# Optimization experiments

Hardware: AMD Instinct MI355X
Metric: run time of the kernel (lower is better)

The kernel has to match this reference:

```python
import jax, jax.numpy as jnp
import numpy as np

P_MIN = 0.8        # minimum cumulative probability mass kept per row
THRESHOLD = 1e-10  # drop matches with probability below this
EPS = 1e-6         # distance clamp (matches dist.clamp(min=1e-6) in backward)

B, N, M, D = 4, 4096, 4096, 3


def setup_inputs() -> dict:
    key = jax.random.key(0)
    kx, ky = jax.random.split(key)
    x = jax.random.normal(kx, (B, N, D), dtype=jnp.float32)
    y = jax.random.normal(ky, (B, M, D), dtype=jnp.float32)
    return {"x": x, "y": y}


def _pairwise_dist(x, y):
    # ||x_i - y_j|| via Gram trick; avoids materializing [B,N,M,D] diff tensor.
    sq = (
        jnp.sum(x * x, axis=-1)[:, :, None]
        + jnp.sum(y * y, axis=-1)[:, None, :]
        - 2.0 * jnp.einsum("bnd,bmd->bnm", x, y)
    )
    return jnp.sqrt(jnp.maximum(sq, EPS * EPS))  # [B, N, M]


def _sparse_match_weights(d):
    # Row-wise soft matching probabilities over targets j.
    p = jax.nn.softmax(-d, axis=-1)  # [B, N, M]
    # Keep the most-probable entries per row until cumulative mass reaches P_MIN
    # (the dense, jit-friendly equivalent of the COO compaction in the kernel).
    order = jnp.argsort(-p, axis=-1)
    p_sorted = jnp.take_along_axis(p, order, axis=-1)
    csum = jnp.cumsum(p_sorted, axis=-1)
    keep_sorted = (csum - p_sorted) < P_MIN  # include entry that crosses P_MIN
    inv = jnp.argsort(order, axis=-1)
    keep = jnp.take_along_axis(keep_sorted, inv, axis=-1)
    return jnp.where(keep & (p > THRESHOLD), p, 0.0)  # sparse COO values, dense layout


def reference(x, y):
    d = _pairwise_dist(x, y)                     # [B, N, M]
    w = jax.lax.stop_gradient(_sparse_match_weights(d))  # weights are constants in bwd
    loss = jnp.sum(w * d)                        # scalar matching loss
    return loss
```

## Files before the change

kernel.cpp:

```cpp
#include <hip/hip_runtime.h>


#define MCOLS 4096
#define KPT   64
#define WPB   4
#define P_MIN 0.8f

template <int CTRL, int RM, int BM, bool BC>
__device__ __forceinline__ float dpp_mov0(float x) {
    return __int_as_float(__builtin_amdgcn_update_dpp(
        0, __float_as_int(x), CTRL, RM, BM, BC));
}
__device__ __forceinline__ float dppSum(float v) {
    v += dpp_mov0<0x111, 0xF, 0xF, true >(v);
    v += dpp_mov0<0x112, 0xF, 0xF, true >(v);
    v += dpp_mov0<0x114, 0xF, 0xF, true >(v);
    v += dpp_mov0<0x118, 0xF, 0xF, true >(v);
    v += dpp_mov0<0x142, 0xA, 0xF, false>(v);
    v += dpp_mov0<0x143, 0xC, 0xF, false>(v);
    return __int_as_float(__builtin_amdgcn_readlane(__float_as_int(v), 63));
}
__device__ __forceinline__ float dppMax(float v) {
    v = fmaxf(v, dpp_mov0<0x111, 0xF, 0xF, true >(v));
    v = fmaxf(v, dpp_mov0<0x112, 0xF, 0xF, true >(v));
    v = fmaxf(v, dpp_mov0<0x114, 0xF, 0xF, true >(v));
    v = fmaxf(v, dpp_mov0<0x118, 0xF, 0xF, true >(v));
    v = fmaxf(v, dpp_mov0<0x142, 0xA, 0xF, false>(v));
    v = fmaxf(v, dpp_mov0<0x143, 0xC, 0xF, false>(v));
    return __int_as_float(__builtin_amdgcn_readlane(__float_as_int(v), 63));
}

__global__ __launch_bounds__(WPB * 64) void apml_row_wave(
        const float* __restrict__ x, const float* __restrict__ y,
        float* __restrict__ out) {
    __shared__ __align__(16) float scomp[WPB * 256];
    __shared__ float wacc[WPB];

    const int tid  = threadIdx.x;
    const int wid  = tid >> 6;
    const int lane = tid & 63;
    const int row  = blockIdx.x * WPB + wid;
    const int b    = row >> 12;

    const float x0 = x[row * 3 + 0];
    const float x1 = x[row * 3 + 1];
    const float x2 = x[row * 3 + 2];
    const float* yb = y + (size_t)b * MCOLS * 3;

    float p[KPT];
    float zl = 0.0f, pml = 0.0f;
    #pragma unroll
    for (int k = 0; k < KPT; ++k) {
        const int j = k * 64 + lane;
        const float y0 = yb[j * 3 + 0];
        const float y1 = yb[j * 3 + 1];
        const float y2 = yb[j * 3 + 2];
        const float dx = x0 - y0, dy = x1 - y1, dz = x2 - y2;
        const float sq = fmaxf(dx * dx + dy * dy + dz * dz, 1e-12f);
        const float pk = __expf(-sqrtf(sq));
        p[k] = pk;
        zl  += pk;
        pml  = fmaxf(pml, pk);
    }
    const float Z    = dppSum(zl);
    const float pmax = dppMax(pml);
    const float target = P_MIN * Z;
    const float pTop = __uint_as_float(__float_as_uint(pmax) + 1u);

    float ssl = 0.0f, ssh = pTop;
    {
        float eGl = 16.0f * dppSum(p[0] + p[1] + p[2] + p[3]);
        float eGh = 0.0f;
        for (int it = 0; it < 5; ++it) {
            float s;
            if (it & 1) {
                s = 0.5f * (ssl + ssh);
            } else {
                const float den = fmaxf(eGl - eGh, 1e-30f);
                s = ssl + (ssh - ssl) * ((eGl - target) / den);
            }
            if (!(s > ssl && s < ssh)) s = 0.5f * (ssl + ssh);
            if (!(s > ssl && s < ssh)) break;
            float m = 0.0f;
            #pragma unroll
            for (int q = 0; q < 4; ++q) m += (p[q] >= s) ? p[q] : 0.0f;
            m = 16.0f * dppSum(m);
            if (m >= target) { ssl = s; eGl = m; }
            else             { ssh = s; eGh = m; }
        }
    }

    float sl = 0.0f, sh = pTop;
    float Gl = Z,    Gh = 0.0f;
    int   Cl = MCOLS, Ch = 0;

    for (int it = 0; it < 12 && (Cl - Ch) > 256; ++it) {
        float s;
        if      (it == 0) s = ssl;
        else if (it == 1) s = ssh;
        else if (it & 1)  s = 0.5f * (sl + sh);
        else {
            const float den = fmaxf(Gl - Gh, 1e-30f);
            s = sl + (sh - sl) * ((Gl - target) / den);
        }
        if (!(s > sl && s < sh)) s = 0.5f * (sl + sh);
        if (!(s > sl && s < sh)) break;

        float m = 0.0f;
        int   c = 0;
        #pragma unroll
        for (int k = 0; k < KPT; ++k) {
            const bool ge = (p[k] >= s);
            m += ge ? p[k] : 0.0f;
            c += (int)__popcll(__ballot(ge));
        }
        m = dppSum(m);
        if (m >= target) { sl = s; Gl = m; Cl = c; }
        else             { sh = s; Gh = m; Ch = c; }
    }

    int C = 0;
    #pragma unroll
    for (int k = 0; k < KPT; ++k) {
        const bool band = (p[k] >= sl) && (p[k] < sh);
        const unsigned long long mk = __ballot(band);
        if (band) {
            const unsigned mlo = (unsigned)mk, mhi = (unsigned)(mk >> 32);
            const int within = __builtin_amdgcn_mbcnt_hi(
                                   mhi, __builtin_amdgcn_mbcnt_lo(mlo, 0));
            const int pos = C + within;
            if (pos < 256) scomp[wid * 256 + pos] = p[k];
        }
        C += (int)__popcll(mk);
    }
    __builtin_amdgcn_s_waitcnt(0);
    float cp[4];
    bool  cv[4];
    #pragma unroll
    for (int q = 0; q < 4; ++q) {
        const int idx = q * 64 + lane;
        cv[q] = (idx < C) && (idx < 256);
        cp[q] = cv[q] ? scomp[wid * 256 + idx] : 0.0f;
    }

    float pstar, mb = 0.0f;
    int   cnt = 1;
    bool  haveTie;

    if (C > 256) {
        pstar = (sl > 0.0f) ? __uint_as_float(__float_as_uint(sl) - 1u) : 0.0f;
        haveTie = false;
    } else {
        float lo_s = sl, hi_s = sh, lo_G = Gl, hi_G = Gh;
        int   lo_C = Cl, hi_C = Ch;
        for (int it = 0; it < 10 && (lo_C - hi_C) > 2; ++it) {
            float s;
            if (it & 1) {
                s = 0.5f * (lo_s + hi_s);
            } else {
                const float den = fmaxf(lo_G - hi_G, 1e-30f);
                s = lo_s + (hi_s - lo_s) * ((lo_G - target) / den);
            }
            if (!(s > lo_s && s < hi_s)) s = 0.5f * (lo_s + hi_s);
            if (!(s > lo_s && s < hi_s)) break;

            float m = 0.0f;
            int   c = Ch;
            #pragma unroll
            for (int q = 0; q < 4; ++q) {
                const bool ge = cv[q] && (cp[q] >= s);
                m += ge ? cp[q] : 0.0f;
                c += (int)__popcll(__ballot(ge));
            }
            m = Gh + dppSum(m);
            if (m >= target) { lo_s = s; lo_G = m; lo_C = c; }
            else             { hi_s = s; hi_G = m; hi_C = c; }
        }

        float scur = hi_s, M = hi_G;
        bool ok = false;
        pstar = lo_s;
        for (int e = 0; e < 16; ++e) {
            float vl = 0.0f;
            #pragma unroll
            for (int q = 0; q < 4; ++q)
                vl = fmaxf(vl, (cv[q] && cp[q] < scur) ? cp[q] : 0.0f);
            const float v = dppMax(vl);
            if (!(v > 0.0f)) break;
            int cvn = 0;
            #pragma unroll
            for (int q = 0; q < 4; ++q)
                cvn += (int)__popcll(__ballot(cv[q] && (cp[q] == v)));
            const float Mn = M + v * (float)cvn;
            if (Mn >= target) { pstar = v; mb = M; cnt = cvn; ok = true; break; }
            M = Mn; scur = v;
        }
        haveTie = ok;
        if (!ok) {
            pstar = (lo_s > 0.0f) ? __uint_as_float(__float_as_uint(lo_s) - 1u)
                                  : 0.0f;
        }
    }

    float spd = 0.0f;
    #pragma unroll
    for (int k = 0; k < KPT; ++k) {
        const float t = (p[k] > pstar) ? p[k] : 1.0f;
        spd += t * (-__logf(t));
    }
    spd = dppSum(spd);

    if (lane == 0) {
        float tie = 0.0f;
        if (haveTie) {
            const float R = (target - mb) / pstar;
            int q = (int)ceilf(R);
            if (q < 1) q = 1;
            if (q > cnt) q = cnt;
            tie = (float)q * pstar * (-__logf(pstar));
        }
        wacc[wid] = (spd + tie) / Z;
    }
    __syncthreads();
    if (tid == 0) {
        atomicAdd(out, wacc[0] + wacc[1] + wacc[2] + wacc[3]);
    }
}

extern "C" void kernel_launch(void* const* d_in, const int* in_sizes, int n_in,
                              void* d_out, int out_size, void* d_ws, size_t ws_size,
                              hipStream_t stream) {
    const float* x = (const float*)d_in[0];
    const float* y = (const float*)d_in[1];
    float* out = (float*)d_out;

    const int nrows = in_sizes[0] / 3;
    const int nblocks = nrows / WPB;

    hipMemsetAsync(out, 0, sizeof(float), stream);
    apml_row_wave<<<nblocks, WPB * 64, 0, stream>>>(x, y, out);
}
```

Before: 166.9 us.

## Batch initial threshold probes, split reductions into ILP chains, replace atomics with reduce kernel

The first two threshold probes of the mass search now run in a single pass over the 64 per-lane values, with both dual DPP sums interleaved. The remaining probe loop and the running max use four independent accumulators to shorten dependency chains. The global atomicAdd plus memset is replaced by per-block partials written to workspace and a separate single-block reduction kernel, which adds a second launch but removes atomic contention and the memset. The intent is fewer serialized reduction steps per row and cheaper final accumulation.

```diff
diff --git a/kernel.cpp b/kernel.cpp
--- a/kernel.cpp
+++ b/kernel.cpp
@@ -20,6 +20,16 @@
     v += dpp_mov0<0x143, 0xC, 0xF, false>(v);
     return __int_as_float(__builtin_amdgcn_readlane(__float_as_int(v), 63));
 }
+__device__ __forceinline__ void dppSum2(float& a, float& b) {
+    a += dpp_mov0<0x111, 0xF, 0xF, true >(a); b += dpp_mov0<0x111, 0xF, 0xF, true >(b);
+    a += dpp_mov0<0x112, 0xF, 0xF, true >(a); b += dpp_mov0<0x112, 0xF, 0xF, true >(b);
+    a += dpp_mov0<0x114, 0xF, 0xF, true >(a); b += dpp_mov0<0x114, 0xF, 0xF, true >(b);
+    a += dpp_mov0<0x118, 0xF, 0xF, true >(a); b += dpp_mov0<0x118, 0xF, 0xF, true >(b);
+    a += dpp_mov0<0x142, 0xA, 0xF, false>(a); b += dpp_mov0<0x142, 0xA, 0xF, false>(b);
+    a += dpp_mov0<0x143, 0xC, 0xF, false>(a); b += dpp_mov0<0x143, 0xC, 0xF, false>(b);
+    a = __int_as_float(__builtin_amdgcn_readlane(__float_as_int(a), 63));
+    b = __int_as_float(__builtin_amdgcn_readlane(__float_as_int(b), 63));
+}
 __device__ __forceinline__ float dppMax(float v) {
     v = fmaxf(v, dpp_mov0<0x111, 0xF, 0xF, true >(v));
     v = fmaxf(v, dpp_mov0<0x112, 0xF, 0xF, true >(v));
@@ -32,7 +42,7 @@
 
 __global__ __launch_bounds__(WPB * 64) void apml_row_wave(
         const float* __restrict__ x, const float* __restrict__ y,
-        float* __restrict__ out) {
+        float* __restrict__ partial, float* __restrict__ out) {
     __shared__ __align__(16) float scomp[WPB * 256];
     __shared__ float wacc[WPB];
 
@@ -48,7 +58,8 @@
     const float* yb = y + (size_t)b * MCOLS * 3;
 
     float p[KPT];
-    float zl = 0.0f, pml = 0.0f;
+    float zl = 0.0f;
+    float pm0 = 0.0f, pm1 = 0.0f, pm2 = 0.0f, pm3 = 0.0f;
     #pragma unroll
     for (int k = 0; k < KPT; ++k) {
         const int j = k * 64 + lane;
@@ -60,10 +71,13 @@
         const float pk = __expf(-sqrtf(sq));
         p[k] = pk;
         zl  += pk;
-        pml  = fmaxf(pml, pk);
+        if      ((k & 3) == 0) pm0 = fmaxf(pm0, pk);
+        else if ((k & 3) == 1) pm1 = fmaxf(pm1, pk);
+        else if ((k & 3) == 2) pm2 = fmaxf(pm2, pk);
+        else                   pm3 = fmaxf(pm3, pk);
     }
     const float Z    = dppSum(zl);
-    const float pmax = dppMax(pml);
+    const float pmax = dppMax(fmaxf(fmaxf(pm0, pm1), fmaxf(pm2, pm3)));
     const float target = P_MIN * Z;
     const float pTop = __uint_as_float(__float_as_uint(pmax) + 1u);
 
@@ -93,28 +107,49 @@
     float sl = 0.0f, sh = pTop;
     float Gl = Z,    Gh = 0.0f;
     int   Cl = MCOLS, Ch = 0;
-
-    for (int it = 0; it < 12 && (Cl - Ch) > 256; ++it) {
+    {
+        float ml = 0.0f, mh = 0.0f;
+        int   cl_ = 0,   ch_ = 0;
+        #pragma unroll
+        for (int k = 0; k < KPT; ++k) {
+            const float pk = p[k];
+            const bool gl = (pk >= ssl);
+            const bool gh = (pk >= ssh);
+            ml += gl ? pk : 0.0f; cl_ += (int)__popcll(__ballot(gl));
+            mh += gh ? pk : 0.0f; ch_ += (int)__popcll(__ballot(gh));
+        }
+        dppSum2(ml, mh);
+        if (ml >= target) { sl = ssl; Gl = ml; Cl = cl_; }
+        else              { sh = ssl; Gh = ml; Ch = cl_; }
+        if (mh >= target) { sl = ssh; Gl = mh; Cl = ch_; }
+        else if (ssh < sh){ sh = ssh; Gh = mh; Ch = ch_; }
+    }
+
+    for (int it = 0; it < 10 && (Cl - Ch) > 256; ++it) {
         float s;
-        if      (it == 0) s = ssl;
-        else if (it == 1) s = ssh;
-        else if (it & 1)  s = 0.5f * (sl + sh);
-        else {
+        if (it & 1) {
+            s = 0.5f * (sl + sh);
+        } else {
             const float den = fmaxf(Gl - Gh, 1e-30f);
             s = sl + (sh - sl) * ((Gl - target) / den);
         }
         if (!(s > sl && s < sh)) s = 0.5f * (sl + sh);
         if (!(s > sl && s < sh)) break;
 
-        float m = 0.0f;
+        float m0 = 0.0f, m1 = 0.0f, m2 = 0.0f, m3 = 0.0f;
         int   c = 0;
         #pragma unroll
-        for (int k = 0; k < KPT; ++k) {
-            const bool ge = (p[k] >= s);
-            m += ge ? p[k] : 0.0f;
-            c += (int)__popcll(__ballot(ge));
-        }
-        m = dppSum(m);
+        for (int k = 0; k < KPT; k += 4) {
+            const bool g0 = (p[k]     >= s);
+            const bool g1 = (p[k + 1] >= s);
+            const bool g2 = (p[k + 2] >= s);
+            const bool g3 = (p[k + 3] >= s);
+            m0 += g0 ? p[k]     : 0.0f; c += (int)__popcll(__ballot(g0));
+            m1 += g1 ? p[k + 1] : 0.0f; c += (int)__popcll(__ballot(g1));
+            m2 += g2 ? p[k + 2] : 0.0f; c += (int)__popcll(__ballot(g2));
+            m3 += g3 ? p[k + 3] : 0.0f; c += (int)__popcll(__ballot(g3));
+        }
+        const float m = dppSum((m0 + m1) + (m2 + m3));
         if (m >= target) { sl = s; Gl = m; Cl = c; }
         else             { sh = s; Gh = m; Ch = c; }
     }
@@ -223,7 +258,30 @@
     }
     __syncthreads();
     if (tid == 0) {
-        atomicAdd(out, wacc[0] + wacc[1] + wacc[2] + wacc[3]);
+        const float v = wacc[0] + wacc[1] + wacc[2] + wacc[3];
+        if (partial) partial[blockIdx.x] = v;
+        else         atomicAdd(out, v);
+    }
+}
+
+__global__ __launch_bounds__(1024) void apml_reduce(
+        const float* __restrict__ partial, float* __restrict__ out, int n) {
+    __shared__ float s[16];
+    const int t = threadIdx.x;
+    float a = 0.0f;
+    #pragma unroll
+    for (int q = 0; q < 4; ++q) {
+        const int i = t * 4 + q;
+        a += (i < n) ? partial[i] : 0.0f;
+    }
+    a = dppSum(a);
+    if ((t & 63) == 0) s[t >> 6] = a;
+    __syncthreads();
+    if (t == 0) {
+        float r = 0.0f;
+        #pragma unroll
+        for (int w = 0; w < 16; ++w) r += s[w];
+        out[0] = r;
     }
 }
 
@@ -237,6 +295,12 @@
     const int nrows = in_sizes[0] / 3;
     const int nblocks = nrows / WPB;
 
-    hipMemsetAsync(out, 0, sizeof(float), stream);
-    apml_row_wave<<<nblocks, WPB * 64, 0, stream>>>(x, y, out);
-}
+    if (d_ws && ws_size >= (size_t)nblocks * sizeof(float) && nblocks <= 4096) {
+        float* partial = (float*)d_ws;
+        apml_row_wave<<<nblocks, WPB * 64, 0, stream>>>(x, y, partial, out);
+        apml_reduce<<<1, 1024, 0, stream>>>(partial, out, nblocks);
+    } else {
+        hipMemsetAsync(out, 0, sizeof(float), stream);
+        apml_row_wave<<<nblocks, WPB * 64, 0, stream>>>(x, y, nullptr, out);
+    }
+}
```

Result: no change. 166.1 us (-0.5%).
